# Kernel tuning notes

Measured on AMD Instinct MI355X. Metric: run time of the kernel, lower is better.

## Reference

```python
import jax, jax.numpy as jnp
from jax import lax
import numpy as np

IN, H, L, OUT = 64, 1024, 2, 1
B, T = 64, 512


def setup_inputs() -> dict:
    key = jax.random.key(0)
    ks = jax.random.split(key, 12)
    stdv = 1.0 / np.sqrt(H)
    u = lambda k, shape: jax.random.uniform(k, shape, jnp.float32, -stdv, stdv)
    return {
        "x": jax.random.normal(ks[0], (B, T, IN), jnp.float32),
        "h_state": jax.random.normal(ks[1], (L, B, H), jnp.float32),
        "W_ih0": u(ks[2], (H, IN)),
        "W_hh0": u(ks[3], (H, H)),
        "b_ih0": u(ks[4], (H,)),
        "b_hh0": u(ks[5], (H,)),
        "W_ih1": u(ks[6], (H, H)),
        "W_hh1": u(ks[7], (H, H)),
        "b_ih1": u(ks[8], (H,)),
        "b_hh1": u(ks[9], (H,)),
        "W_out": u(ks[10], (OUT, H)),
        "b_out": u(ks[11], (OUT,)),
    }


def _rnn_layer(inp, h0, W_ih, W_hh, b_ih, b_hh):
    # Precompute input projection for all timesteps as one big GEMM: [B,T,H]
    xp = jnp.einsum('bti,hi->bth', inp, W_ih) + b_ih + b_hh

    def step(h, xt):  # xt: [B,H]
        h_new = jnp.tanh(xt + h @ W_hh.T)
        return h_new, h_new

    h_last, outs = lax.scan(step, h0, xp.transpose(1, 0, 2))  # outs: [T,B,H]
    return outs.transpose(1, 0, 2), h_last


def reference(x, h_state, W_ih0, W_hh0, b_ih0, b_hh0, W_ih1, W_hh1, b_ih1, b_hh1, W_out, b_out):
    r1, h1 = _rnn_layer(x, h_state[0], W_ih0, W_hh0, b_ih0, b_hh0)
    r2, h2 = _rnn_layer(r1, h_state[1], W_ih1, W_hh1, b_ih1, b_hh1)
    proj = jnp.einsum('bth,oh->bto', r2, W_out) + b_out  # [B,T,1]
    out = proj[:, 0:1, :]  # module keeps only t=0, re-expanded to [B,1,1]
    h_new = jnp.stack([h1, h2], axis=0)  # [L,B,H]
    return out, h_new
```

## Files before the change

kernel.cpp:

```cpp
#include <hip/hip_runtime.h>
#include <hip/hip_bf16.h>


typedef float f32x4 __attribute__((ext_vector_type(4)));
typedef _Float16 half8 __attribute__((ext_vector_type(8)));

#define T_STEPS 512
#define STEPS 513

#define CTR_OFF   0
#define XT_OFF    16384
#define H1_OFF    (XT_OFF + 4194304)
#define H2_OFF    (H1_OFF + 262144)
#define H2T0_OFF  (H2_OFF + 262144)

__device__ inline float tanh_fast(float z) {
  z = fminf(20.f, fmaxf(-20.f, z));
  float e = __expf(2.f * z);
  return (e - 1.f) / (e + 1.f);
}

__device__ inline half8 ldw8(const float* p) {
  half8 r;
#pragma unroll
  for (int i = 0; i < 8; ++i) r[i] = (_Float16)p[i];
  return r;
}

__device__ inline half8 ldh8_coh(const _Float16* p) {
  union { unsigned long long q[2]; half8 h; } u;
  unsigned long long* a = (unsigned long long*)p;
  u.q[0] = __hip_atomic_load(a,     __ATOMIC_RELAXED, __HIP_MEMORY_SCOPE_AGENT);
  u.q[1] = __hip_atomic_load(a + 1, __ATOMIC_RELAXED, __HIP_MEMORY_SCOPE_AGENT);
  return u.h;
}

__device__ inline void sth_coh(_Float16* p, float v) {
  union { _Float16 h; unsigned short u; } cv;
  cv.h = (_Float16)v;
  __hip_atomic_store((unsigned short*)p, cv.u, __ATOMIC_RELAXED, __HIP_MEMORY_SCOPE_AGENT);
}

__global__ void prep_x(const float* __restrict__ x, _Float16* __restrict__ xt) {
  int i = blockIdx.x * 256 + threadIdx.x;
  int j = i & 7;
  int row = (i >> 3) & 15;
  int kgv = (i >> 7) & 7;
  int gg = (i >> 10) & 3;
  int t = i >> 12;
  int b = gg * 16 + row;
  xt[i] = (_Float16)x[(b * 512 + t) * 64 + kgv * 8 + j];
}

__global__ void prep_h(const float* __restrict__ hs, _Float16* __restrict__ h1b,
                       _Float16* __restrict__ h2b, char* __restrict__ wsbase) {
  int i = blockIdx.x * 256 + threadIdx.x;
  int j = i & 7;
  int row = (i >> 3) & 15;
  int kgv = (i >> 7) & 127;
  int gg = (i >> 14) & 3;
  int l = i >> 16;
  int b = gg * 16 + row;
  int h = kgv * 8 + j;
  float v = hs[(size_t)l * 65536 + b * 1024 + h];
  _Float16* dst = l ? h2b : h1b;
  dst[(size_t)(4 + gg) * 16384 + (kgv * 16 + row) * 8 + j] = (_Float16)v;
  if (i < 256) *(unsigned*)(wsbase + CTR_OFF + (size_t)i * 64) = 0u;
}

__global__ __launch_bounds__(256, 1) void rnn_persist(
    const float* __restrict__ Wih0, const float* __restrict__ Whh0,
    const float* __restrict__ bih0, const float* __restrict__ bhh0,
    const float* __restrict__ Wih1, const float* __restrict__ Whh1,
    const float* __restrict__ bih1, const float* __restrict__ bhh1,
    const float* __restrict__ Wout, const float* __restrict__ bout,
    float* __restrict__ out, char* __restrict__ ws) {
  __shared__ float pcL1[256];
  __shared__ float pcL2[256];

  const int bid = blockIdx.x;
  const int g = bid >> 6;
  const int cu = bid & 63;
  const int tid = threadIdx.x;
  const int wave = tid >> 6;
  const int lane = tid & 63;
  const int col = lane & 15;
  const int kg = lane >> 4;

  unsigned* flags = (unsigned*)(ws + CTR_OFF);
  const _Float16* xt = (const _Float16*)(ws + XT_OFF);
  _Float16* h1b = (_Float16*)(ws + H1_OFF);
  _Float16* h2b = (_Float16*)(ws + H2_OFF);
  float* h2t0 = (float*)(ws + H2T0_OFF);

  const int c = cu * 16 + col;

  half8 bw[32];
  float bias = 0.f;
  if (wave == 0) {
#pragma unroll
    for (int f = 0; f < 17; ++f) {
      int k0 = f * 32 + kg * 8;
      const float* p = (k0 < 64) ? (Wih0 + c * 64 + k0) : (Whh0 + c * 1024 + (k0 - 64));
      bw[f] = ldw8(p);
    }
    bias = bih0[c] + bhh0[c];
  } else if (wave == 1) {
#pragma unroll
    for (int f = 0; f < 17; ++f) {
      int k0 = (f + 17) * 32 + kg * 8 - 64;
      bw[f] = ldw8(Whh0 + c * 1024 + k0);
    }
  } else if (wave == 2) {
#pragma unroll
    for (int f = 0; f < 32; ++f) {
      int k0 = f * 32 + kg * 8;
      bw[f] = ldw8(Wih1 + c * 1024 + k0);
    }
    bias = bih1[c] + bhh1[c];
  } else {
#pragma unroll
    for (int f = 0; f < 32; ++f) {
      int k0 = f * 32 + kg * 8;
      bw[f] = ldw8(Whh1 + c * 1024 + k0);
    }
  }

  for (int s = 0; s < STEPS; ++s) {
    const bool l1act = (s < T_STEPS);
    const bool l2act = (s >= 1);
    const _Float16* h1rd = h1b + (size_t)(((s + 1) & 1) * 4 + g) * 16384;
    const _Float16* h2rd = h2b + (size_t)(((s) & 1) * 4 + g) * 16384;
    _Float16* h1wr = h1b + (size_t)(((s) & 1) * 4 + g) * 16384;
    _Float16* h2wr = h2b + (size_t)(((s + 1) & 1) * 4 + g) * 16384;

    f32x4 acc = {0.f, 0.f, 0.f, 0.f};
    if (wave == 0) {
      if (l1act) {
        const _Float16* xsrc = xt + (size_t)(s * 4 + g) * 1024;
#pragma unroll
        for (int f = 0; f < 17; ++f) {
          half8 a = (f < 2) ? *(const half8*)(xsrc + f * 512 + lane * 8)
                            : ldh8_coh(h1rd + (f - 2) * 512 + lane * 8);
          acc = __builtin_amdgcn_mfma_f32_16x16x32_f16(a, bw[f], acc, 0, 0, 0);
        }
      }
    } else if (wave == 1) {
      if (l1act) {
#pragma unroll
        for (int f = 0; f < 17; ++f) {
          half8 a = ldh8_coh(h1rd + (f + 15) * 512 + lane * 8);
          acc = __builtin_amdgcn_mfma_f32_16x16x32_f16(a, bw[f], acc, 0, 0, 0);
        }
#pragma unroll
        for (int r = 0; r < 4; ++r) pcL1[(kg * 4 + r) * 16 + col] = acc[r];
      }
    } else if (wave == 2) {
      if (l2act) {
#pragma unroll
        for (int f = 0; f < 32; ++f) {
          half8 a = ldh8_coh(h1rd + f * 512 + lane * 8);
          acc = __builtin_amdgcn_mfma_f32_16x16x32_f16(a, bw[f], acc, 0, 0, 0);
        }
      }
    } else {
      if (l2act) {
#pragma unroll
        for (int f = 0; f < 32; ++f) {
          half8 a = ldh8_coh(h2rd + f * 512 + lane * 8);
          acc = __builtin_amdgcn_mfma_f32_16x16x32_f16(a, bw[f], acc, 0, 0, 0);
        }
#pragma unroll
        for (int r = 0; r < 4; ++r) pcL2[(kg * 4 + r) * 16 + col] = acc[r];
      }
    }
    __syncthreads();

    if (wave == 0 && l1act) {
#pragma unroll
      for (int r = 0; r < 4; ++r) {
        int row = kg * 4 + r;
        float z = acc[r] + pcL1[row * 16 + col] + bias;
        float h = tanh_fast(z);
        sth_coh(h1wr + ((cu * 2 + (col >> 3)) * 16 + row) * 8 + (col & 7), h);
        if (s == T_STEPS - 1) out[64 + (g * 16 + row) * 1024 + c] = h;
      }
    }
    if (wave == 2 && l2act) {
#pragma unroll
      for (int r = 0; r < 4; ++r) {
        int row = kg * 4 + r;
        float z = acc[r] + pcL2[row * 16 + col] + bias;
        float h = tanh_fast(z);
        sth_coh(h2wr + ((cu * 2 + (col >> 3)) * 16 + row) * 8 + (col & 7), h);
        if (s == 1)
          __hip_atomic_store((unsigned*)(h2t0 + (size_t)(g * 16 + row) * 1024 + c),
                             __float_as_uint(h), __ATOMIC_RELAXED,
                             __HIP_MEMORY_SCOPE_AGENT);
        if (s == STEPS - 1) out[64 + 65536 + (g * 16 + row) * 1024 + c] = h;
      }
    }
    __syncthreads();

    if (tid == 0)
      __hip_atomic_store(flags + (size_t)(g * 64 + cu) * 16, (unsigned)(s + 1),
                         __ATOMIC_RELAXED, __HIP_MEMORY_SCOPE_AGENT);
    if (tid < 64) {
      unsigned* f = flags + (size_t)(g * 64 + tid) * 16;
      unsigned spins = 0;
      while (__hip_atomic_load(f, __ATOMIC_RELAXED, __HIP_MEMORY_SCOPE_AGENT) <
             (unsigned)(s + 1)) {
        __builtin_amdgcn_s_sleep(1);
        if (++spins > (1u << 20)) break;
      }
    }
    __syncthreads();
  }

  if (cu == 0) {
    const int b = tid >> 4, seg = tid & 15;
    const float* hrow = h2t0 + (size_t)(g * 16 + b) * 1024 + seg * 64;
    const float* wrow = Wout + seg * 64;
    float sum = 0.f;
#pragma unroll
    for (int i = 0; i < 64; ++i) {
      unsigned u = __hip_atomic_load((unsigned*)(hrow + i), __ATOMIC_RELAXED,
                                     __HIP_MEMORY_SCOPE_AGENT);
      sum += __uint_as_float(u) * wrow[i];
    }
    sum += __shfl_xor(sum, 1);
    sum += __shfl_xor(sum, 2);
    sum += __shfl_xor(sum, 4);
    sum += __shfl_xor(sum, 8);
    if (seg == 0) out[g * 16 + b] = sum + bout[0];
  }
}

extern "C" void kernel_launch(void* const* d_in, const int* in_sizes, int n_in,
                              void* d_out, int out_size, void* d_ws, size_t ws_size,
                              hipStream_t stream) {
  const float* x    = (const float*)d_in[0];
  const float* hs   = (const float*)d_in[1];
  const float* Wih0 = (const float*)d_in[2];
  const float* Whh0 = (const float*)d_in[3];
  const float* bih0 = (const float*)d_in[4];
  const float* bhh0 = (const float*)d_in[5];
  const float* Wih1 = (const float*)d_in[6];
  const float* Whh1 = (const float*)d_in[7];
  const float* bih1 = (const float*)d_in[8];
  const float* bhh1 = (const float*)d_in[9];
  const float* Wout = (const float*)d_in[10];
  const float* bout = (const float*)d_in[11];
  float* out = (float*)d_out;
  char* ws = (char*)d_ws;

  _Float16* xt  = (_Float16*)(ws + XT_OFF);
  _Float16* h1b = (_Float16*)(ws + H1_OFF);
  _Float16* h2b = (_Float16*)(ws + H2_OFF);

  prep_x<<<8192, 256, 0, stream>>>(x, xt);
  prep_h<<<512, 256, 0, stream>>>(hs, h1b, h2b, ws);
  rnn_persist<<<256, 256, 0, stream>>>(Wih0, Whh0, bih0, bhh0,
                                       Wih1, Whh1, bih1, bhh1,
                                       Wout, bout, out, ws);
}
```

Measured before the change: 2.575 ms.

## Merge column tiles into 512-thread blocks and stage hidden state in LDS

Each block now holds two 16-column tiles (8 waves) instead of one, halving the grid to 128 blocks and the number of flags each group polls per step. Every step, the whole block first copies the h1/h2 slices it needs from global memory into shared memory with coherent loads, and the MFMA loops then read their A operands from LDS. This removes duplicated global/L2 reads across waves and cuts the barrier fan-in. In exchange it adds an extra __syncthreads and a serialized staging phase each step, uses only half as many CUs, and relies on 64KB of LDS per block.

Result: faster. 2.295 ms (-10.9%).

```diff
diff --git a/kernel.cpp b/kernel.cpp
--- a/kernel.cpp
+++ b/kernel.cpp
@@ -68,21 +68,24 @@
   if (i < 256) *(unsigned*)(wsbase + CTR_OFF + (size_t)i * 64) = 0u;
 }
 
-__global__ __launch_bounds__(256, 1) void rnn_persist(
+__global__ __launch_bounds__(512, 1) void rnn_persist(
     const float* __restrict__ Wih0, const float* __restrict__ Whh0,
     const float* __restrict__ bih0, const float* __restrict__ bhh0,
     const float* __restrict__ Wih1, const float* __restrict__ Whh1,
     const float* __restrict__ bih1, const float* __restrict__ bhh1,
     const float* __restrict__ Wout, const float* __restrict__ bout,
     float* __restrict__ out, char* __restrict__ ws) {
-  __shared__ float pcL1[256];
-  __shared__ float pcL2[256];
+  __shared__ _Float16 h1s[16384];
+  __shared__ _Float16 h2s[16384];
+  __shared__ float pcL1[2][256];
+  __shared__ float pcL2[2][256];
 
   const int bid = blockIdx.x;
-  const int g = bid >> 6;
-  const int cu = bid & 63;
+  const int g = bid >> 5;
+  const int wgi = bid & 31;
   const int tid = threadIdx.x;
-  const int wave = tid >> 6;
+  const int quad = tid >> 8;
+  const int wq = (tid >> 6) & 3;
   const int lane = tid & 63;
   const int col = lane & 15;
   const int kg = lane >> 4;
@@ -93,11 +96,12 @@
   _Float16* h2b = (_Float16*)(ws + H2_OFF);
   float* h2t0 = (float*)(ws + H2T0_OFF);
 
+  const int cu = wgi * 2 + quad;
   const int c = cu * 16 + col;
 
   half8 bw[32];
   float bias = 0.f;
-  if (wave == 0) {
+  if (wq == 0) {
 #pragma unroll
     for (int f = 0; f < 17; ++f) {
       int k0 = f * 32 + kg * 8;
@@ -105,13 +109,13 @@
       bw[f] = ldw8(p);
     }
     bias = bih0[c] + bhh0[c];
-  } else if (wave == 1) {
+  } else if (wq == 1) {
 #pragma unroll
     for (int f = 0; f < 17; ++f) {
       int k0 = (f + 17) * 32 + kg * 8 - 64;
       bw[f] = ldw8(Whh0 + c * 1024 + k0);
     }
-  } else if (wave == 2) {
+  } else if (wq == 2) {
 #pragma unroll
     for (int f = 0; f < 32; ++f) {
       int k0 = f * 32 + kg * 8;
@@ -134,32 +138,40 @@
     _Float16* h1wr = h1b + (size_t)(((s) & 1) * 4 + g) * 16384;
     _Float16* h2wr = h2b + (size_t)(((s + 1) & 1) * 4 + g) * 16384;
 
+#pragma unroll
+    for (int it = 0; it < 4; ++it)
+      *(half8*)&h1s[(it * 512 + tid) * 8] = ldh8_coh(h1rd + (size_t)(it * 512 + tid) * 8);
+#pragma unroll
+    for (int it = 0; it < 4; ++it)
+      *(half8*)&h2s[(it * 512 + tid) * 8] = ldh8_coh(h2rd + (size_t)(it * 512 + tid) * 8);
+    __syncthreads();
+
     f32x4 acc = {0.f, 0.f, 0.f, 0.f};
-    if (wave == 0) {
+    if (wq == 0) {
       if (l1act) {
         const _Float16* xsrc = xt + (size_t)(s * 4 + g) * 1024;
 #pragma unroll
         for (int f = 0; f < 17; ++f) {
           half8 a = (f < 2) ? *(const half8*)(xsrc + f * 512 + lane * 8)
-                            : ldh8_coh(h1rd + (f - 2) * 512 + lane * 8);
-          acc = __builtin_amdgcn_mfma_f32_16x16x32_f16(a, bw[f], acc, 0, 0, 0);
-        }
-      }
-    } else if (wave == 1) {
+                            : *(const half8*)&h1s[(f - 2) * 512 + lane * 8];
+          acc = __builtin_amdgcn_mfma_f32_16x16x32_f16(a, bw[f], acc, 0, 0, 0);
+        }
+      }
+    } else if (wq == 1) {
       if (l1act) {
 #pragma unroll
         for (int f = 0; f < 17; ++f) {
-          half8 a = ldh8_coh(h1rd + (f + 15) * 512 + lane * 8);
-          acc = __builtin_amdgcn_mfma_f32_16x16x32_f16(a, bw[f], acc, 0, 0, 0);
-        }
-#pragma unroll
-        for (int r = 0; r < 4; ++r) pcL1[(kg * 4 + r) * 16 + col] = acc[r];
-      }
-    } else if (wave == 2) {
+          half8 a = *(const half8*)&h1s[(f + 15) * 512 + lane * 8];
+          acc = __builtin_amdgcn_mfma_f32_16x16x32_f16(a, bw[f], acc, 0, 0, 0);
+        }
+#pragma unroll
+        for (int r = 0; r < 4; ++r) pcL1[quad][(kg * 4 + r) * 16 + col] = acc[r];
+      }
+    } else if (wq == 2) {
       if (l2act) {
 #pragma unroll
         for (int f = 0; f < 32; ++f) {
-          half8 a = ldh8_coh(h1rd + f * 512 + lane * 8);
+          half8 a = *(const half8*)&h1s[f * 512 + lane * 8];
           acc = __builtin_amdgcn_mfma_f32_16x16x32_f16(a, bw[f], acc, 0, 0, 0);
         }
       }
@@ -167,30 +179,30 @@
       if (l2act) {
 #pragma unroll
         for (int f = 0; f < 32; ++f) {
-          half8 a = ldh8_coh(h2rd + f * 512 + lane * 8);
-          acc = __builtin_amdgcn_mfma_f32_16x16x32_f16(a, bw[f], acc, 0, 0, 0);
-        }
-#pragma unroll
-        for (int r = 0; r < 4; ++r) pcL2[(kg * 4 + r) * 16 + col] = acc[r];
-      }
-    }
-    __syncthreads();
-
-    if (wave == 0 && l1act) {
+          half8 a = *(const half8*)&h2s[f * 512 + lane * 8];
+          acc = __builtin_amdgcn_mfma_f32_16x16x32_f16(a, bw[f], acc, 0, 0, 0);
+        }
+#pragma unroll
+        for (int r = 0; r < 4; ++r) pcL2[quad][(kg * 4 + r) * 16 + col] = acc[r];
+      }
+    }
+    __syncthreads();
+
+    if (wq == 0 && l1act) {
 #pragma unroll
       for (int r = 0; r < 4; ++r) {
         int row = kg * 4 + r;
-        float z = acc[r] + pcL1[row * 16 + col] + bias;
+        float z = acc[r] + pcL1[quad][row * 16 + col] + bias;
         float h = tanh_fast(z);
         sth_coh(h1wr + ((cu * 2 + (col >> 3)) * 16 + row) * 8 + (col & 7), h);
         if (s == T_STEPS - 1) out[64 + (g * 16 + row) * 1024 + c] = h;
       }
     }
-    if (wave == 2 && l2act) {
+    if (wq == 2 && l2act) {
 #pragma unroll
       for (int r = 0; r < 4; ++r) {
         int row = kg * 4 + r;
-        float z = acc[r] + pcL2[row * 16 + col] + bias;
+        float z = acc[r] + pcL2[quad][row * 16 + col] + bias;
         float h = tanh_fast(z);
         sth_coh(h2wr + ((cu * 2 + (col >> 3)) * 16 + row) * 8 + (col & 7), h);
         if (s == 1)
@@ -203,10 +215,10 @@
     __syncthreads();
 
     if (tid == 0)
-      __hip_atomic_store(flags + (size_t)(g * 64 + cu) * 16, (unsigned)(s + 1),
+      __hip_atomic_store(flags + (size_t)(g * 32 + wgi) * 16, (unsigned)(s + 1),
                          __ATOMIC_RELAXED, __HIP_MEMORY_SCOPE_AGENT);
-    if (tid < 64) {
-      unsigned* f = flags + (size_t)(g * 64 + tid) * 16;
+    if (tid < 32) {
+      unsigned* f = flags + (size_t)(g * 32 + tid) * 16;
       unsigned spins = 0;
       while (__hip_atomic_load(f, __ATOMIC_RELAXED, __HIP_MEMORY_SCOPE_AGENT) <
              (unsigned)(s + 1)) {
@@ -217,7 +229,7 @@
     __syncthreads();
   }
 
-  if (cu == 0) {
+  if (wgi == 0 && tid < 256) {
     const int b = tid >> 4, seg = tid & 15;
     const float* hrow = h2t0 + (size_t)(g * 16 + b) * 1024 + seg * 64;
     const float* wrow = Wout + seg * 64;
@@ -260,7 +272,7 @@
 
   prep_x<<<8192, 256, 0, stream>>>(x, xt);
   prep_h<<<512, 256, 0, stream>>>(hs, h1b, h2b, ws);
-  rnn_persist<<<256, 256, 0, stream>>>(Wih0, Whh0, bih0, bhh0,
+  rnn_persist<<<128, 512, 0, stream>>>(Wih0, Whh0, bih0, bhh0,
                                        Wih1, Whh1, bih1, bhh1,
                                        Wout, bout, out, ws);
 }
```

## Decouple layer pipelines with per-layer flags and warp-specialized waves

Applied to the files above, without the earlier changes.

Replaces the single per-step barrier (block-wide syncthreads plus one global flag set) with separate global flag arrays for layer 1 and layer 2. Three specialized waves now run their own loops: wave 0 runs the full layer-1 recurrence, wave 1 computes the layer-2 input projection, and wave 2 computes layer 2's recurrent term and output. The waves hand off through double-buffered shared memory and intra-workgroup atomic flags. The aim is to let layer 1 run ahead of layer 2 and to remove the block-wide stalls, at the cost of wave 0 doing twice the MFMA chain serially and more complex spin-based handshakes.

Result: slower. 2.966 ms (+15.2%).

```diff
diff --git a/kernel.cpp b/kernel.cpp
--- a/kernel.cpp
+++ b/kernel.cpp
@@ -6,13 +6,15 @@
 typedef _Float16 half8 __attribute__((ext_vector_type(8)));
 
 #define T_STEPS 512
-#define STEPS 513
-
-#define CTR_OFF   0
-#define XT_OFF    16384
+
+#define FH1_OFF   0
+#define FH2_OFF   16384
+#define XT_OFF    32768
 #define H1_OFF    (XT_OFF + 4194304)
 #define H2_OFF    (H1_OFF + 262144)
 #define H2T0_OFF  (H2_OFF + 262144)
+
+#define SPIN_CAP (1u << 20)
 
 __device__ inline float tanh_fast(float z) {
   z = fminf(20.f, fmaxf(-20.f, z));
@@ -39,6 +41,18 @@
   union { _Float16 h; unsigned short u; } cv;
   cv.h = (_Float16)v;
   __hip_atomic_store((unsigned short*)p, cv.u, __ATOMIC_RELAXED, __HIP_MEMORY_SCOPE_AGENT);
+}
+
+__device__ inline void poll_flags(int* base, int lane, int t) {
+  int* f = base + (size_t)lane * 16;
+  unsigned spins = 0;
+  for (;;) {
+    int v = __hip_atomic_load(f, __ATOMIC_RELAXED, __HIP_MEMORY_SCOPE_AGENT);
+    if (__all(v >= t)) break;
+    __builtin_amdgcn_s_sleep(1);
+    if (++spins > SPIN_CAP) break;
+  }
+  asm volatile("" ::: "memory");
 }
 
 __global__ void prep_x(const float* __restrict__ x, _Float16* __restrict__ xt) {
@@ -65,18 +79,21 @@
   float v = hs[(size_t)l * 65536 + b * 1024 + h];
   _Float16* dst = l ? h2b : h1b;
   dst[(size_t)(4 + gg) * 16384 + (kgv * 16 + row) * 8 + j] = (_Float16)v;
-  if (i < 256) *(unsigned*)(wsbase + CTR_OFF + (size_t)i * 64) = 0u;
-}
-
-__global__ __launch_bounds__(256, 1) void rnn_persist(
+  if (i < 512) *(int*)(wsbase + (size_t)i * 64) = (i >= 256) ? 1 : 0;
+}
+
+__global__ __launch_bounds__(192, 1) void rnn_persist(
     const float* __restrict__ Wih0, const float* __restrict__ Whh0,
     const float* __restrict__ bih0, const float* __restrict__ bhh0,
     const float* __restrict__ Wih1, const float* __restrict__ Whh1,
     const float* __restrict__ bih1, const float* __restrict__ bhh1,
     const float* __restrict__ Wout, const float* __restrict__ bout,
     float* __restrict__ out, char* __restrict__ ws) {
-  __shared__ float pcL1[256];
-  __shared__ float pcL2[256];
+  __shared__ float pcA[256];
+  __shared__ float pcB[256];
+  __shared__ int pcflag;
+  __shared__ int ackflag;
+  __shared__ int h1done;
 
   const int bid = blockIdx.x;
   const int g = bid >> 6;
@@ -87,7 +104,8 @@
   const int col = lane & 15;
   const int kg = lane >> 4;
 
-  unsigned* flags = (unsigned*)(ws + CTR_OFF);
+  int* fh1 = (int*)(ws + FH1_OFF) + (size_t)g * 64 * 16;
+  int* fh2 = (int*)(ws + FH2_OFF) + (size_t)g * 64 * 16;
   const _Float16* xt = (const _Float16*)(ws + XT_OFF);
   _Float16* h1b = (_Float16*)(ws + H1_OFF);
   _Float16* h2b = (_Float16*)(ws + H2_OFF);
@@ -95,11 +113,13 @@
 
   const int c = cu * 16 + col;
 
-  half8 bw[32];
+  if (tid == 0) { pcflag = 0; ackflag = 0; h1done = 0; }
+
+  half8 bw[34];
   float bias = 0.f;
   if (wave == 0) {
 #pragma unroll
-    for (int f = 0; f < 17; ++f) {
+    for (int f = 0; f < 34; ++f) {
       int k0 = f * 32 + kg * 8;
       const float* p = (k0 < 64) ? (Wih0 + c * 64 + k0) : (Whh0 + c * 1024 + (k0 - 64));
       bw[f] = ldw8(p);
@@ -107,132 +127,125 @@
     bias = bih0[c] + bhh0[c];
   } else if (wave == 1) {
 #pragma unroll
-    for (int f = 0; f < 17; ++f) {
-      int k0 = (f + 17) * 32 + kg * 8 - 64;
-      bw[f] = ldw8(Whh0 + c * 1024 + k0);
-    }
-  } else if (wave == 2) {
-#pragma unroll
-    for (int f = 0; f < 32; ++f) {
-      int k0 = f * 32 + kg * 8;
-      bw[f] = ldw8(Wih1 + c * 1024 + k0);
-    }
+    for (int f = 0; f < 32; ++f) bw[f] = ldw8(Wih1 + c * 1024 + f * 32 + kg * 8);
+  } else {
+#pragma unroll
+    for (int f = 0; f < 32; ++f) bw[f] = ldw8(Whh1 + c * 1024 + f * 32 + kg * 8);
     bias = bih1[c] + bhh1[c];
-  } else {
-#pragma unroll
-    for (int f = 0; f < 32; ++f) {
-      int k0 = f * 32 + kg * 8;
-      bw[f] = ldw8(Whh1 + c * 1024 + k0);
-    }
   }
-
-  for (int s = 0; s < STEPS; ++s) {
-    const bool l1act = (s < T_STEPS);
-    const bool l2act = (s >= 1);
-    const _Float16* h1rd = h1b + (size_t)(((s + 1) & 1) * 4 + g) * 16384;
-    const _Float16* h2rd = h2b + (size_t)(((s) & 1) * 4 + g) * 16384;
-    _Float16* h1wr = h1b + (size_t)(((s) & 1) * 4 + g) * 16384;
-    _Float16* h2wr = h2b + (size_t)(((s + 1) & 1) * 4 + g) * 16384;
-
-    f32x4 acc = {0.f, 0.f, 0.f, 0.f};
-    if (wave == 0) {
-      if (l1act) {
-        const _Float16* xsrc = xt + (size_t)(s * 4 + g) * 1024;
-#pragma unroll
-        for (int f = 0; f < 17; ++f) {
-          half8 a = (f < 2) ? *(const half8*)(xsrc + f * 512 + lane * 8)
-                            : ldh8_coh(h1rd + (f - 2) * 512 + lane * 8);
-          acc = __builtin_amdgcn_mfma_f32_16x16x32_f16(a, bw[f], acc, 0, 0, 0);
-        }
-      }
-    } else if (wave == 1) {
-      if (l1act) {
-#pragma unroll
-        for (int f = 0; f < 17; ++f) {
-          half8 a = ldh8_coh(h1rd + (f + 15) * 512 + lane * 8);
-          acc = __builtin_amdgcn_mfma_f32_16x16x32_f16(a, bw[f], acc, 0, 0, 0);
-        }
-#pragma unroll
-        for (int r = 0; r < 4; ++r) pcL1[(kg * 4 + r) * 16 + col] = acc[r];
-      }
-    } else if (wave == 2) {
-      if (l2act) {
-#pragma unroll
-        for (int f = 0; f < 32; ++f) {
-          half8 a = ldh8_coh(h1rd + f * 512 + lane * 8);
-          acc = __builtin_amdgcn_mfma_f32_16x16x32_f16(a, bw[f], acc, 0, 0, 0);
-        }
-      }
-    } else {
-      if (l2act) {
-#pragma unroll
-        for (int f = 0; f < 32; ++f) {
-          half8 a = ldh8_coh(h2rd + f * 512 + lane * 8);
-          acc = __builtin_amdgcn_mfma_f32_16x16x32_f16(a, bw[f], acc, 0, 0, 0);
-        }
-#pragma unroll
-        for (int r = 0; r < 4; ++r) pcL2[(kg * 4 + r) * 16 + col] = acc[r];
-      }
-    }
-    __syncthreads();
-
-    if (wave == 0 && l1act) {
+  __syncthreads();
+
+  if (wave == 0) {
+    for (int s = 0; s < T_STEPS; ++s) {
+      if (s > 0) poll_flags(fh1, lane, s);
+      const _Float16* h1rd = h1b + (size_t)(((s + 1) & 1) * 4 + g) * 16384;
+      _Float16* h1wr = h1b + (size_t)((s & 1) * 4 + g) * 16384;
+      const _Float16* xsrc = xt + (size_t)(s * 4 + g) * 1024;
+      f32x4 acc = {0.f, 0.f, 0.f, 0.f};
+#pragma unroll
+      for (int f = 0; f < 34; ++f) {
+        half8 a = (f < 2) ? *(const half8*)(xsrc + f * 512 + lane * 8)
+                          : ldh8_coh(h1rd + (f - 2) * 512 + lane * 8);
+        acc = __builtin_amdgcn_mfma_f32_16x16x32_f16(a, bw[f], acc, 0, 0, 0);
+      }
 #pragma unroll
       for (int r = 0; r < 4; ++r) {
         int row = kg * 4 + r;
-        float z = acc[r] + pcL1[row * 16 + col] + bias;
-        float h = tanh_fast(z);
+        float h = tanh_fast(acc[r] + bias);
         sth_coh(h1wr + ((cu * 2 + (col >> 3)) * 16 + row) * 8 + (col & 7), h);
         if (s == T_STEPS - 1) out[64 + (g * 16 + row) * 1024 + c] = h;
       }
-    }
-    if (wave == 2 && l2act) {
+      asm volatile("s_waitcnt vmcnt(0)" ::: "memory");
+      {
+        unsigned spins = 0;
+        while (__hip_atomic_load(&h1done, __ATOMIC_ACQUIRE,
+                                 __HIP_MEMORY_SCOPE_WORKGROUP) < s) {
+          __builtin_amdgcn_s_sleep(1);
+          if (++spins > SPIN_CAP) break;
+        }
+      }
+      if (lane == 0)
+        __hip_atomic_store(fh1 + (size_t)cu * 16, s + 1,
+                           __ATOMIC_RELAXED, __HIP_MEMORY_SCOPE_AGENT);
+    }
+  } else if (wave == 1) {
+    for (int s = 1; s <= T_STEPS; ++s) {
+      {
+        unsigned spins = 0;
+        while (__hip_atomic_load(&ackflag, __ATOMIC_ACQUIRE,
+                                 __HIP_MEMORY_SCOPE_WORKGROUP) < s - 2) {
+          __builtin_amdgcn_s_sleep(1);
+          if (++spins > SPIN_CAP) break;
+        }
+      }
+      poll_flags(fh1, lane, s);
+      const _Float16* h1rd = h1b + (size_t)(((s + 1) & 1) * 4 + g) * 16384;
+      f32x4 acc = {0.f, 0.f, 0.f, 0.f};
+#pragma unroll
+      for (int f = 0; f < 32; ++f) {
+        half8 a = ldh8_coh(h1rd + f * 512 + lane * 8);
+        acc = __builtin_amdgcn_mfma_f32_16x16x32_f16(a, bw[f], acc, 0, 0, 0);
+      }
+      __hip_atomic_store(&h1done, s, __ATOMIC_RELEASE,
+                         __HIP_MEMORY_SCOPE_WORKGROUP);
+      float* pc = (s & 1) ? pcA : pcB;
+#pragma unroll
+      for (int r = 0; r < 4; ++r) pc[(kg * 4 + r) * 16 + col] = acc[r];
+      __hip_atomic_store(&pcflag, s, __ATOMIC_RELEASE,
+                         __HIP_MEMORY_SCOPE_WORKGROUP);
+    }
+  } else {
+    for (int s = 1; s <= T_STEPS; ++s) {
+      poll_flags(fh2, lane, s);
+      const _Float16* h2rd = h2b + (size_t)((s & 1) * 4 + g) * 16384;
+      _Float16* h2wr = h2b + (size_t)(((s + 1) & 1) * 4 + g) * 16384;
+      f32x4 acc = {0.f, 0.f, 0.f, 0.f};
+#pragma unroll
+      for (int f = 0; f < 32; ++f) {
+        half8 a = ldh8_coh(h2rd + f * 512 + lane * 8);
+        acc = __builtin_amdgcn_mfma_f32_16x16x32_f16(a, bw[f], acc, 0, 0, 0);
+      }
+      {
+        unsigned spins = 0;
+        while (__hip_atomic_load(&pcflag, __ATOMIC_ACQUIRE,
+                                 __HIP_MEMORY_SCOPE_WORKGROUP) < s) {
+          __builtin_amdgcn_s_sleep(1);
+          if (++spins > SPIN_CAP) break;
+        }
+      }
+      const float* pc = (s & 1) ? pcA : pcB;
 #pragma unroll
       for (int r = 0; r < 4; ++r) {
         int row = kg * 4 + r;
-        float z = acc[r] + pcL2[row * 16 + col] + bias;
-        float h = tanh_fast(z);
+        float h = tanh_fast(acc[r] + pc[row * 16 + col] + bias);
         sth_coh(h2wr + ((cu * 2 + (col >> 3)) * 16 + row) * 8 + (col & 7), h);
         if (s == 1)
           __hip_atomic_store((unsigned*)(h2t0 + (size_t)(g * 16 + row) * 1024 + c),
                              __float_as_uint(h), __ATOMIC_RELAXED,
                              __HIP_MEMORY_SCOPE_AGENT);
-        if (s == STEPS - 1) out[64 + 65536 + (g * 16 + row) * 1024 + c] = h;
-      }
-    }
-    __syncthreads();
-
-    if (tid == 0)
-      __hip_atomic_store(flags + (size_t)(g * 64 + cu) * 16, (unsigned)(s + 1),
-                         __ATOMIC_RELAXED, __HIP_MEMORY_SCOPE_AGENT);
-    if (tid < 64) {
-      unsigned* f = flags + (size_t)(g * 64 + tid) * 16;
-      unsigned spins = 0;
-      while (__hip_atomic_load(f, __ATOMIC_RELAXED, __HIP_MEMORY_SCOPE_AGENT) <
-             (unsigned)(s + 1)) {
-        __builtin_amdgcn_s_sleep(1);
-        if (++spins > (1u << 20)) break;
-      }
-    }
-    __syncthreads();
-  }
-
-  if (cu == 0) {
-    const int b = tid >> 4, seg = tid & 15;
-    const float* hrow = h2t0 + (size_t)(g * 16 + b) * 1024 + seg * 64;
-    const float* wrow = Wout + seg * 64;
-    float sum = 0.f;
-#pragma unroll
-    for (int i = 0; i < 64; ++i) {
-      unsigned u = __hip_atomic_load((unsigned*)(hrow + i), __ATOMIC_RELAXED,
-                                     __HIP_MEMORY_SCOPE_AGENT);
-      sum += __uint_as_float(u) * wrow[i];
-    }
-    sum += __shfl_xor(sum, 1);
-    sum += __shfl_xor(sum, 2);
-    sum += __shfl_xor(sum, 4);
-    sum += __shfl_xor(sum, 8);
-    if (seg == 0) out[g * 16 + b] = sum + bout[0];
+        if (s == T_STEPS) out[64 + 65536 + (g * 16 + row) * 1024 + c] = h;
+      }
+      __hip_atomic_store(&ackflag, s, __ATOMIC_RELEASE,
+                         __HIP_MEMORY_SCOPE_WORKGROUP);
+      asm volatile("s_waitcnt vmcnt(0)" ::: "memory");
+      if (lane == 0)
+        __hip_atomic_store(fh2 + (size_t)cu * 16, s + 1,
+                           __ATOMIC_RELAXED, __HIP_MEMORY_SCOPE_AGENT);
+    }
+    if (cu == 0) {
+      const int b = lane & 15, q = lane >> 4;
+      const float* hrow = h2t0 + (size_t)(g * 16 + b) * 1024 + q * 256;
+      const float* wrow = Wout + q * 256;
+      float sum = 0.f;
+      for (int i = 0; i < 256; ++i) {
+        unsigned u = __hip_atomic_load((unsigned*)(hrow + i), __ATOMIC_RELAXED,
+                                       __HIP_MEMORY_SCOPE_AGENT);
+        sum += __uint_as_float(u) * wrow[i];
+      }
+      sum += __shfl_xor(sum, 16);
+      sum += __shfl_xor(sum, 32);
+      if (q == 0) out[g * 16 + b] = sum + bout[0];
+    }
   }
 }
 
@@ -260,7 +273,7 @@
 
   prep_x<<<8192, 256, 0, stream>>>(x, xt);
   prep_h<<<512, 256, 0, stream>>>(hs, h1b, h2b, ws);
-  rnn_persist<<<256, 256, 0, stream>>>(Wih0, Whh0, bih0, bhh0,
+  rnn_persist<<<256, 192, 0, stream>>>(Wih0, Whh0, bih0, bhh0,
                                        Wih1, Whh1, bih1, bhh1,
                                        Wout, bout, out, ws);
 }
```
